# Performance work log

Hardware: AMD Instinct MI355X
Metric: run time of the kernel (lower is better)

Reference implementation:

```python
import jax, jax.numpy as jnp
import numpy as np

B, C, NQ, K, H, CAM, FFN = 2, 128, 200, 24000, 8, 16, 256

def setup_inputs() -> dict:
    key = jax.random.key(0)
    ks = jax.random.split(key, 32)
    def n(i, shape, scale=1.0):
        return jax.random.normal(ks[i], shape, dtype=jnp.float32) * scale
    return {
        "query_feat": n(0, (B, C, NQ)),
        "key_feat": n(1, (B, C, K)),
        "query_pos": jax.random.uniform(ks[2], (B, NQ, 2), dtype=jnp.float32),
        "key_pos": jax.random.uniform(ks[3], (B, K, 2), dtype=jnp.float32),
        "query_size": jax.random.uniform(ks[4], (B, NQ, 2), dtype=jnp.float32, minval=0.02, maxval=0.3),
        "cam_info": n(5, (B, CAM, K)),
        "Wproj_q": n(6, (C, C), 0.05), "Wproj_k": n(7, (C, C), 0.05),
        "Wq_pos1": n(8, (2, C), 0.5), "Wq_pos2": n(9, (C, C), 0.05),
        "Wk_pos1": n(10, (2, C), 0.5), "Wk_pos2": n(11, (C, C), 0.05),
        "Wsq": n(12, (C, C), 0.05), "Wsk": n(13, (C, C), 0.05),
        "Wsv": n(14, (C, C), 0.05), "Wso": n(15, (C, C), 0.05),
        "Wcq": n(16, (C, C), 0.05), "Wck": n(17, (C, C), 0.05),
        "Wcv": n(18, (C, C), 0.05), "Wco": n(19, (C, C), 0.05),
        "Wffn1": n(20, (C, FFN), 0.05), "bffn1": jnp.zeros((FFN,), jnp.float32),
        "Wffn2": n(21, (FFN, C), 0.05), "bffn2": jnp.zeros((C,), jnp.float32),
        "cam_w1": n(22, (CAM, C), 0.1), "cam_w2": n(23, (C, C), 0.05), "cam_w3": n(24, (C, C), 0.05),
    }

def _ln(x):
    m = x.mean(-1, keepdims=True)
    v = x.var(-1, keepdims=True)
    return (x - m) * jax.lax.rsqrt(v + 1e-5)

def _mha(q, k, v, Wq, Wk, Wv, Wo, bias=None):
    b, nq, c = q.shape
    dh = c // H
    qh = (q @ Wq).reshape(b, nq, H, dh)
    kh = (k @ Wk).reshape(b, k.shape[1], H, dh)
    vh = (v @ Wv).reshape(b, v.shape[1], H, dh)
    s = jnp.einsum('bqhd,bkhd->bhqk', qh, kh) * (1.0 / np.sqrt(dh))
    if bias is not None:
        s = s + bias[:, None]  # SMCA gaussian modulation, shared over heads
    a = jax.nn.softmax(s, axis=-1)
    o = jnp.einsum('bhqk,bkhd->bqhd', a, vh).reshape(b, nq, c)
    return o @ Wo

def reference(query_feat, key_feat, query_pos, key_pos, query_size, cam_info,
              Wproj_q, Wproj_k, Wq_pos1, Wq_pos2, Wk_pos1, Wk_pos2,
              Wsq, Wsk, Wsv, Wso, Wcq, Wck, Wcv, Wco,
              Wffn1, bffn1, Wffn2, bffn2, cam_w1, cam_w2, cam_w3):
    # 1x1-conv projections (img_projection / pts_projection)
    q = jnp.einsum('bcn,cd->bnd', query_feat, Wproj_q)   # [B,NQ,C]
    kf = jnp.einsum('bck,cd->bkd', key_feat, Wproj_k)    # [B,K,C]
    mu = cam_info.mean(axis=(0, 2), keepdims=True)
    var = cam_info.var(axis=(0, 2), keepdims=True)
    cb = (cam_info - mu) * jax.lax.rsqrt(var + 1e-5)     # [B,16,K]
    h = jax.nn.relu(jnp.einsum('bck,cd->bdk', cb, cam_w1))
    h = jax.nn.relu(jnp.einsum('bck,cd->bdk', h, cam_w2))
    gate = jax.nn.sigmoid(jnp.einsum('bck,cd->bdk', h, cam_w3))  # [B,C,K]
    kf = kf * gate.transpose(0, 2, 1)
    # learned position embeddings (MLP on normalized 2D coords)
    qpe = jax.nn.relu(query_pos @ Wq_pos1) @ Wq_pos2     # [B,NQ,C]
    kpe = jax.nn.relu(key_pos @ Wk_pos1) @ Wk_pos2       # [B,K,C]
    # self-attention over queries
    x = q
    xs = x + qpe
    x = _ln(x + _mha(xs, xs, x, Wsq, Wsk, Wsv, Wso))
    # SMCA gaussian attention bias: -|p_k - p_q|^2 / (2 sigma^2) per axis
    sigma = query_size * 0.5 + 1e-2                      # [B,NQ,2]
    diff = key_pos[:, None] - query_pos[:, :, None]      # [B,NQ,K,2]
    bias = -jnp.sum(diff * diff / (2.0 * (sigma * sigma)[:, :, None]), axis=-1)  # [B,NQ,K]
    # cross-attention with SMCA modulation
    x = _ln(x + _mha(x + qpe, kf + kpe, kf, Wcq, Wck, Wcv, Wco, bias))
    # FFN
    x = _ln(x + (jax.nn.relu(x @ Wffn1 + bffn1) @ Wffn2 + bffn2))
    return x  # [B,NQ,C]
```

## Files before the change

kernel.cpp:

```cpp
#include <hip/hip_runtime.h>
#include <math.h>

#define BB 2
#define CC 128
#define NQ 200
#define NQP 224
#define KK 24000
#define NH 8
#define DH 16
#define NCAM 16
#define NFFN 256

#define NSEG 50
#define TPS 15
#define NGRP (BB*NSEG)
#define SLOTX 13

#define TK 64
#define NPS (BB*NQP)
#define NQB (BB*NQ)

#define LOG2E 1.44269504f

#if __has_builtin(__builtin_amdgcn_exp2f)
#define EXP2(x) __builtin_amdgcn_exp2f(x)
#else
#define EXP2(x) exp2f(x)
#endif

#define O_MU    0
#define O_RSTD  16
#define O_SINV  32
#define O_CP    1024
#define O_Q0    2048
#define O_QPE   (O_Q0  + BB*NQ*CC)
#define O_XS    (O_QPE + BB*NQ*CC)
#define O_SQ    (O_XS  + BB*NQ*CC)
#define O_SK    (O_SQ  + BB*NQ*CC)
#define O_SV    (O_SK  + BB*NQ*CC)
#define O_SO    (O_SV  + BB*NQ*CC)
#define O_X1    (O_SO  + BB*NQ*CC)
#define O_OH    (O_X1  + BB*NQ*CC)
#define O_PART  (O_OH  + BB*NQ*CC)
#define O_BF    (O_PART + BB*NH*NSEG*NQP*18)

#define U_KH   0
#define U_VH   (BB*KK*CC)
#define U_FT   (2*BB*KK*CC)
#define U_CT   (3*BB*KK*CC)
#define U_W    (3*BB*KK*CC + BB*KK*32)
#define U_QW   (U_W + 4096 + 6*16384)
#define U_ONES (U_QW + BB*NQP*CC)
#define U_WX   (U_ONES + KK + 64)

typedef __attribute__((ext_vector_type(8))) short bfrag8;
typedef __attribute__((ext_vector_type(4))) float f32x4;
typedef __attribute__((ext_vector_type(16))) float f32x16;

__device__ __forceinline__ unsigned short f2bf(float x) {
    unsigned u = __float_as_uint(x);
    u += 0x7fffu + ((u >> 16) & 1u);
    return (unsigned short)(u >> 16);
}
__device__ __forceinline__ float bf2f(unsigned short h) {
    return __uint_as_float(((unsigned)h) << 16);
}
__device__ __forceinline__ unsigned cvtpk_bf16(float lo, float hi) {
    unsigned r;
    asm volatile("v_cvt_pk_bf16_f32 %0, %1, %2" : "=v"(r) : "v"(lo), "v"(hi));
    return r;
}
__device__ __forceinline__ void pl32swap(unsigned &a, unsigned &b) {
    asm volatile("v_permlane32_swap_b32 %0, %1" : "+v"(a), "+v"(b));
}

__device__ __forceinline__ float lnorm512(float x, int t, float* rs, float* rs2, float* col) {
    if (t < 128) { rs[t] = x; rs2[t] = x*x; }
    __syncthreads();
    if (t < 64) {
        float v  = rs[t]  + rs[t+64];
        float v2 = rs2[t] + rs2[t+64];
#pragma unroll
        for (int off = 32; off > 0; off >>= 1) {
            v  += __shfl_down(v,  off);
            v2 += __shfl_down(v2, off);
        }
        if (t == 0) { col[0] = v; col[1] = v2; }
    }
    __syncthreads();
    float mean = col[0] * (1.0f/128.0f);
    float var  = col[1] * (1.0f/128.0f) - mean*mean;
    return (x - mean) * rsqrtf(var + 1e-5f);
}


__global__ __launch_bounds__(512) void k_pre(
    const float* __restrict__ cam,
    const float* __restrict__ cw2, const float* __restrict__ cw3,
    const float* __restrict__ proj, const float* __restrict__ k2,
    const float* __restrict__ ck,  const float* __restrict__ cv,
    const float* __restrict__ cw1,
    unsigned short* __restrict__ wtU, unsigned short* __restrict__ onesU,
    unsigned short* __restrict__ wxU,
    float* __restrict__ ws,
    const float* __restrict__ qf, const float* __restrict__ qpos,
    const float* __restrict__ qsize,
    const float* __restrict__ Wpq, const float* __restrict__ Wp1,
    const float* __restrict__ Wp2,
    const float* __restrict__ Wsq, const float* __restrict__ Wsk,
    const float* __restrict__ Wsv)
{
    __shared__ float r1[256], r2[256];
    __shared__ float qrow[CC], ph[CC], xsr[CC], q0r[CC];
    __shared__ float pA[4*132], pB[4*132], pC[4*132];
    __shared__ float wckL[128*16];
    int t = threadIdx.x;
    if (blockIdx.x < 256) {
        int blk = blockIdx.x;
        int r = blk >> 3;
        int s = blk & 7;
        const float* src = cam + (size_t)r*KK + s*3000;
        float sm = 0.f, s2 = 0.f;
        if (t < 256)
            for (int i = t; i < 3000; i += 256) { float v = src[i]; sm += v; s2 += v*v; }
        if (t < 256) { r1[t] = sm; r2[t] = s2; }
        __syncthreads();
        for (int off = 128; off > 0; off >>= 1) {
            if (t < off) { r1[t] += r1[t+off]; r2[t] += r2[t+off]; }
            __syncthreads();
        }
        if (t == 0) { ws[O_CP + blk*2] = r1[0]; ws[O_CP + blk*2 + 1] = r2[0]; }
    } else if (blockIdx.x < 264) {
        int blk = blockIdx.x - 256;
        if (blk < 6) {
            const float* W = (blk==0)?cw2:(blk==1)?cw3:(blk==2)?proj:(blk==3)?k2:(blk==4)?ck:cv;
            unsigned short* dst = wtU + 4096 + blk*16384;
            for (int i = t; i < 16384; i += 512) {
                int j = i & 7, lx = (i >> 3) & 63, cs = (i >> 9) & 3, w16 = i >> 11;
                int d = w16*16 + (lx & 15);
                int c = cs*32 + (lx >> 4)*8 + j;
                dst[i] = f2bf(W[c*CC + d]);
            }
        } else if (blk == 6) {
            for (int i = t; i < 4096; i += 512) {
                int j = i & 7, lx = (i >> 3) & 63, w16 = i >> 9;
                int d = w16*16 + (lx & 15);
                int c = (lx >> 4)*8 + j;
                wtU[i] = (c < 16) ? f2bf(cw1[c*CC + d]) : (unsigned short)0;
            }
        } else {
            for (int i = t; i < KK + 64; i += 512) onesU[i] = 0x3F80;
        }
    } else if (blockIdx.x < 264 + NQB) {
        int row = blockIdx.x - 264;
        int b = row / NQ, n = row - b*NQ;
        int d = t & 127, p = t >> 7;
        if (t < CC) {
            qrow[t] = qf[((size_t)b*CC + t)*NQ + n];
            float px = qpos[row*2], py = qpos[row*2+1];
            ph[t] = fmaxf(px*Wp1[t] + py*Wp1[CC+t], 0.f);
        }
        if (t < 2) {
            float sg = qsize[row*2 + t]*0.5f + 0.01f;
            ws[O_SINV + row*2 + t] = LOG2E / (2.f * sg * sg);
        }
        __syncthreads();
        {
            float aQ = 0.f, aP = 0.f;
            int c0 = p*32;
#pragma unroll
            for (int c = 0; c < 32; c++) {
                aQ = fmaf(qrow[c0+c], Wpq[(c0+c)*CC + d], aQ);
                aP = fmaf(ph[c0+c],   Wp2[(c0+c)*CC + d], aP);
            }
            pA[p*132 + d] = aQ; pB[p*132 + d] = aP;
        }
        __syncthreads();
        if (t < CC) {
            float q0 = (pA[t] + pA[132+t]) + (pA[264+t] + pA[396+t]);
            float pe = (pB[t] + pB[132+t]) + (pB[264+t] + pB[396+t]);
            ws[O_Q0  + row*CC + t] = q0;
            ws[O_QPE + row*CC + t] = pe;
            q0r[t] = q0;
            xsr[t] = q0 + pe;
        }
        __syncthreads();
        {
            float a = 0.f, k2v = 0.f, v2 = 0.f;
            int c0 = p*32;
#pragma unroll
            for (int c = 0; c < 32; c++) {
                float xv = xsr[c0+c], qv = q0r[c0+c];
                a   = fmaf(xv, Wsq[(c0+c)*CC + d], a);
                k2v = fmaf(xv, Wsk[(c0+c)*CC + d], k2v);
                v2  = fmaf(qv, Wsv[(c0+c)*CC + d], v2);
            }
            pA[p*132 + d] = a; pB[p*132 + d] = k2v; pC[p*132 + d] = v2;
        }
        __syncthreads();
        if (t < CC) {
            ws[O_SQ + row*CC + t] = (pA[t] + pA[132+t]) + (pA[264+t] + pA[396+t]);
            ws[O_SK + row*CC + t] = (pB[t] + pB[132+t]) + (pB[264+t] + pB[396+t]);
            ws[O_SV + row*CC + t] = (pC[t] + pC[132+t]) + (pC[264+t] + pC[396+t]);
        }
    } else {
        int w16 = blockIdx.x - (264 + NQB);
        {
            int e = t >> 2, i0 = (t & 3) * 4;
#pragma unroll
            for (int i = 0; i < 4; i++)
                wckL[e*16 + i0 + i] = ck[(size_t)e*CC + w16*16 + i0 + i];
        }
        __syncthreads();
        {
            int c = t >> 2, dls = (t & 3) * 4;
            const float* wrow = k2 + (size_t)c*CC;
            float acc[4] = {0.f, 0.f, 0.f, 0.f};
            for (int e = 0; e < 128; e++) {
                float w = wrow[e];
#pragma unroll
                for (int i = 0; i < 4; i++)
                    acc[i] = fmaf(w, wckL[e*16 + dls + i], acc[i]);
            }
            int cs = c >> 5, j = c & 7, lhi = ((c >> 3) & 3) * 16;
#pragma unroll
            for (int i = 0; i < 4; i++) {
                int lane = lhi + (dls + i);
                wxU[((w16*4 + cs) << 9) + lane*8 + j] = f2bf(acc[i]);
            }
        }
    }
}


__device__ __forceinline__ int frag_col(int d0, int m) {
    return ((((d0 >> 5) * 4 + ((d0 >> 3) & 3)) * 16 + m) << 3) + (d0 & 7);
}

__device__ __forceinline__ void ld_a4h(bfrag8 a[4], const unsigned short* __restrict__ Wf,
                                       int w16, int l) {
#pragma unroll
    for (int cs = 0; cs < 4; cs++)
        a[cs] = *(const bfrag8*)(Wf + ((w16*4 + cs) << 9) + l*8);
}

__device__ __forceinline__ void mfma_apply4h(const unsigned short* __restrict__ X,
                                             const bfrag8 a[4],
                                             int l, f32x4 acc[4])
{
    const f32x4 z = {0.f, 0.f, 0.f, 0.f};
#pragma unroll
    for (int kt = 0; kt < 4; kt++) acc[kt] = z;
#pragma unroll
    for (int kt = 0; kt < 4; kt++)
#pragma unroll
        for (int cs = 0; cs < 4; cs++) {
            bfrag8 bf = *(const bfrag8*)(X + ((kt*4 + cs) << 9) + l*8);
            acc[kt] = __builtin_amdgcn_mfma_f32_16x16x32_bf16(a[cs], bf, acc[kt], 0, 0, 0);
        }
}

__device__ __forceinline__ void mfma_acc4h(const unsigned short* __restrict__ X,
                                           const bfrag8 a[4],
                                           int l, f32x4 acc[4])
{
#pragma unroll
    for (int kt = 0; kt < 4; kt++)
#pragma unroll
        for (int cs = 0; cs < 4; cs++) {
            bfrag8 bf = *(const bfrag8*)(X + ((kt*4 + cs) << 9) + l*8);
            acc[kt] = __builtin_amdgcn_mfma_f32_16x16x32_bf16(a[cs], bf, acc[kt], 0, 0, 0);
        }
}

__device__ __forceinline__ void mfma_apply1h(const unsigned short* __restrict__ X,
                                             bfrag8 a1, int l, f32x4 acc[4])
{
    const f32x4 z = {0.f, 0.f, 0.f, 0.f};
#pragma unroll
    for (int kt = 0; kt < 4; kt++) acc[kt] = z;
#pragma unroll
    for (int kt = 0; kt < 4; kt++) {
        bfrag8 bf = *(const bfrag8*)(X + (kt << 11) + l*8);
        acc[kt] = __builtin_amdgcn_mfma_f32_16x16x32_bf16(a1, bf, acc[kt], 0, 0, 0);
    }
}

template<bool RELU>
__device__ __forceinline__ void store_tiles_h(unsigned short* __restrict__ Xd,
                                              const f32x4 acc[4], int m, int g, int dbase)
{
    int cp = frag_col(dbase + g*4, m);
#pragma unroll
    for (int kt = 0; kt < 4; kt++) {
        ushort4 pk;
        float v0 = acc[kt][0], v1 = acc[kt][1], v2 = acc[kt][2], v3 = acc[kt][3];
        if (RELU) { v0 = fmaxf(v0,0.f); v1 = fmaxf(v1,0.f); v2 = fmaxf(v2,0.f); v3 = fmaxf(v3,0.f); }
        pk.x = f2bf(v0); pk.y = f2bf(v1); pk.z = f2bf(v2); pk.w = f2bf(v3);
        *(ushort4*)(Xd + (kt << 11) + cp) = pk;
    }
}


__global__ __launch_bounds__(512) void k_chainps(
    const float* __restrict__ key_feat, const float* __restrict__ cam_info,
    const float* __restrict__ key_pos, const float* __restrict__ Wk1,
    const unsigned short* __restrict__ wtU, const unsigned short* __restrict__ wxU,
    unsigned short* __restrict__ khH, unsigned short* __restrict__ vhH,
    const float* __restrict__ Wso, const float* __restrict__ Wcq,
    unsigned short* __restrict__ qwU,
    float* __restrict__ ws)
{
    __shared__ __align__(16) union SM {
        struct {
            unsigned short XA[8192];
            unsigned short XB[8192];
            float w1buf[256];
            float kpx[TK], kpy[TK];
            float cmu[NCAM], crs[NCAM];
        } c;
        struct {
            float sor[CC], qcr[CC], sq[CC];
            float part[4*132];
            float rs[CC], rs2[CC], col[2];
        } s;
    } sm;

    int t = threadIdx.x;

    if (blockIdx.x < NPS) {
        int row = blockIdx.x;
        int b = row / NQP, n = row - b*NQP;
        if (n >= NQ) { if (t < CC) qwU[(size_t)row*CC + t] = 0; return; }
        int rw = b*NQ + n;
        int d = t & 127, p = t >> 7;
        float* sor = sm.s.sor;
        float* qcr = sm.s.qcr;
        float* sq  = sm.s.sq;
        float* part = sm.s.part;
        float* rs = sm.s.rs;
        float* rs2 = sm.s.rs2;
        float* col = sm.s.col;

        if (t < CC) sq[t] = ws[O_SQ + (size_t)rw*CC + t];
        __syncthreads();

        {
            int h = t >> 6;
            int l = t & 63;
            float qv[16];
#pragma unroll
            for (int j = 0; j < 16; j++) qv[j] = sq[h*16 + j];
            float s[4], pexp[4];
            float mloc = -1e30f;
#pragma unroll
            for (int w2 = 0; w2 < 4; w2++) {
                int k = l + w2*64;
                float sv = -1e30f;
                if (k < NQ) {
                    const float* kr = ws + O_SK + ((size_t)(b*NQ + k))*CC + h*16;
                    float a2 = 0.f;
#pragma unroll
                    for (int j = 0; j < 16; j += 4) {
                        float4 kv = *(const float4*)(kr + j);
                        a2 += qv[j]*kv.x + qv[j+1]*kv.y + qv[j+2]*kv.z + qv[j+3]*kv.w;
                    }
                    sv = a2 * 0.25f;
                }
                s[w2] = sv;
                mloc = fmaxf(mloc, sv);
            }
#pragma unroll
            for (int off = 32; off > 0; off >>= 1) mloc = fmaxf(mloc, __shfl_xor(mloc, off));
            float lsum = 0.f;
#pragma unroll
            for (int w2 = 0; w2 < 4; w2++) {
                pexp[w2] = (s[w2] > -1e29f) ? __expf(s[w2] - mloc) : 0.f;
                lsum += pexp[w2];
            }
#pragma unroll
            for (int off = 32; off > 0; off >>= 1) lsum += __shfl_xor(lsum, off);
            float o[16];
#pragma unroll
            for (int j = 0; j < 16; j++) o[j] = 0.f;
#pragma unroll
            for (int w2 = 0; w2 < 4; w2++) {
                int k = l + w2*64;
                if (k < NQ) {
                    const float* vr = ws + O_SV + ((size_t)(b*NQ + k))*CC + h*16;
                    float pw = pexp[w2];
#pragma unroll
                    for (int j = 0; j < 16; j += 4) {
                        float4 vv = *(const float4*)(vr + j);
                        o[j]   = fmaf(pw, vv.x, o[j]);
                        o[j+1] = fmaf(pw, vv.y, o[j+1]);
                        o[j+2] = fmaf(pw, vv.z, o[j+2]);
                        o[j+3] = fmaf(pw, vv.w, o[j+3]);
                    }
                }
            }
#pragma unroll
            for (int j = 0; j < 16; j++) {
#pragma unroll
                for (int off = 32; off > 0; off >>= 1) o[j] += __shfl_xor(o[j], off);
            }
            if (l == 0) {
                float inv = 1.f / lsum;
#pragma unroll
                for (int j = 0; j < 16; j++) sor[h*16 + j] = o[j] * inv;
            }
        }
        __syncthreads();

        {
            float acc = 0.f;
            int c0 = p*32;
#pragma unroll
            for (int c = 0; c < 32; c++) acc = fmaf(sor[c0+c], Wso[(c0+c)*CC + d], acc);
            part[p*132 + d] = acc;
        }
        __syncthreads();
        float x = 0.f;
        if (t < CC) x = ws[O_Q0 + rw*CC + t] + ((part[t] + part[132+t]) + (part[264+t] + part[396+t]));
        x = lnorm512(x, t, rs, rs2, col);
        if (t < CC) {
            ws[O_X1 + rw*CC + t] = x;
            qcr[t] = x + ws[O_QPE + rw*CC + t];
        }
        __syncthreads();
        {
            float acc = 0.f;
            int c0 = p*32;
#pragma unroll
            for (int c = 0; c < 32; c++) acc = fmaf(qcr[c0+c], Wcq[(c0+c)*CC + d], acc);
            part[p*132 + d] = acc;
        }
        __syncthreads();
        if (t < CC) {
            float qh = (part[t] + part[132+t]) + (part[264+t] + part[396+t]);
            qwU[(size_t)row*CC + t] = f2bf(0.25f * LOG2E * qh);
        }
        return;
    }

    unsigned short* XA = sm.c.XA;
    unsigned short* XB = sm.c.XB;
    float* w1buf = sm.c.w1buf;
    float* kpx = sm.c.kpx;
    float* kpy = sm.c.kpy;
    float* cmu = sm.c.cmu;
    float* crs = sm.c.crs;

    int blk = blockIdx.x - NPS;
    int b = blk / (KK/TK);
    int k0 = (blk - b*(KK/TK)) * TK;
    int l = t & 63;
    int m = l & 15, g = l >> 4;
    int w16 = t >> 6;
    int dbase = w16 * 16;

    const unsigned short* WT_CW1  = wtU;
    const unsigned short* WT_CW2  = wtU + 4096;
    const unsigned short* WT_CW3  = wtU + 4096 + 16384;
    const unsigned short* WT_PROJ = wtU + 4096 + 2*16384;
    const unsigned short* WT_CK   = wtU + 4096 + 4*16384;
    const unsigned short* WT_CV   = wtU + 4096 + 5*16384;

    if (t < NCAM) {
        float S = 0.f, S2 = 0.f;
#pragma unroll
        for (int bb2 = 0; bb2 < BB; bb2++)
#pragma unroll
            for (int s = 0; s < 8; s++) {
                int blk2 = ((bb2*NCAM + t) << 3) | s;
                S  += ws[O_CP + blk2*2];
                S2 += ws[O_CP + blk2*2 + 1];
            }
        float mu  = S * (1.0f/(BB*KK));
        float var = S2 * (1.0f/(BB*KK)) - mu*mu;
        cmu[t] = mu;
        crs[t] = rsqrtf(var + 1e-5f);
    }
    __syncthreads();

    if (t < 256) {
        int c = t >> 4;
        int kq = (t & 15) * 4;
        float4 v = *(const float4*)(cam_info + ((size_t)b*NCAM + c)*KK + k0 + kq);
        float mu = cmu[c], rsd = crs[c];
        int ktb = (kq >> 4) << 11;
        int cb  = frag_col(c & ~7, 0) + (c & 7);
        XA[ktb + cb + ((kq  ) & 15)*8] = f2bf((v.x - mu)*rsd);
        XA[ktb + cb + ((kq+1) & 15)*8] = f2bf((v.y - mu)*rsd);
        XA[ktb + cb + ((kq+2) & 15)*8] = f2bf((v.z - mu)*rsd);
        XA[ktb + cb + ((kq+3) & 15)*8] = f2bf((v.w - mu)*rsd);
        {
            int z = t;
            int kt = z >> 6, r = z & 63;
            int gz = 2 + (r >> 5), mz = (r >> 1) & 15, j4 = (r & 1) * 4;
            ushort4 z4 = make_ushort4(0,0,0,0);
            *(ushort4*)(XA + (kt << 11) + (gz*16 + mz)*8 + j4) = z4;
        }
        w1buf[t] = Wk1[t];
    }
    if (t < TK) {
        float2 p = ((const float2*)key_pos)[b*KK + k0 + t];
        kpx[t] = p.x; kpy[t] = p.y;
    }

    bfrag8 a1 = *(const bfrag8*)(WT_CW1 + (w16 << 9) + l*8);
    bfrag8 aA[4], aB[4], aC[4];
    ld_a4h(aA, WT_CW2, w16, l);
    __syncthreads();

    f32x4 acc[4];

    mfma_apply1h(XA, a1, l, acc);
    store_tiles_h<true>(XB, acc, m, g, dbase);
    __syncthreads();
    ld_a4h(aB, WT_CW3, w16, l);

    mfma_apply4h(XB, aA, l, acc);
    store_tiles_h<true>(XA, acc, m, g, dbase);
    __syncthreads();
    ld_a4h(aA, WT_PROJ, w16, l);

    {
        int c = t >> 2, q4 = t & 3;
        const float* src = key_feat + ((size_t)b*CC + c)*KK + k0 + q4*16;
        int base = (q4 << 11) + frag_col(c & ~7, 0) + (c & 7);
#pragma unroll
        for (int qq = 0; qq < 4; qq++) {
            float4 v = ((const float4*)src)[qq];
            int mk = qq*4;
            XB[base + (mk  )*8] = f2bf(v.x);
            XB[base + (mk+1)*8] = f2bf(v.y);
            XB[base + (mk+2)*8] = f2bf(v.z);
            XB[base + (mk+3)*8] = f2bf(v.w);
        }
    }
    mfma_apply4h(XA, aB, l, acc);
    float garr[4][4];
#pragma unroll
    for (int kt = 0; kt < 4; kt++)
#pragma unroll
        for (int r = 0; r < 4; r++)
            garr[kt][r] = 1.f / (1.f + __expf(-acc[kt][r]));
    __syncthreads();
    ld_a4h(aB, WT_CK, w16, l);

    mfma_apply4h(XB, aA, l, acc);
#pragma unroll
    for (int kt = 0; kt < 4; kt++)
#pragma unroll
        for (int r = 0; r < 4; r++)
            acc[kt][r] *= garr[kt][r];
    store_tiles_h<false>(XA, acc, m, g, dbase);
    __syncthreads();
    ld_a4h(aA, WT_CV, w16, l);
    ld_a4h(aC, wxU, w16, l);

    {
        int k = t >> 3, dq = (t & 7) * 16;
        int ktb = (k >> 4) << 11;
        int mk = k & 15;
        float px = kpx[k], py = kpy[k];
        union { unsigned short u[8]; bfrag8 f; } cA, cB;
#pragma unroll
        for (int j = 0; j < 8; j++) {
            cA.u[j] = f2bf(fmaxf(px*w1buf[dq+j]   + py*w1buf[128+dq+j],   0.f));
            cB.u[j] = f2bf(fmaxf(px*w1buf[dq+8+j] + py*w1buf[128+dq+8+j], 0.f));
        }
        *(bfrag8*)(XB + ktb + frag_col(dq,     mk)) = cA.f;
        *(bfrag8*)(XB + ktb + frag_col(dq + 8, mk)) = cB.f;
    }
    __syncthreads();

    mfma_apply4h(XA, aB, l, acc);
    mfma_acc4h(XB, aC, l, acc);
#pragma unroll
    for (int kt = 0; kt < 4; kt++) {
        int k = k0 + kt*16 + m;
        ushort4 pk;
        pk.x = f2bf(acc[kt][0]); pk.y = f2bf(acc[kt][1]);
        pk.z = f2bf(acc[kt][2]); pk.w = f2bf(acc[kt][3]);
        *(ushort4*)(khH + (((size_t)(b*NH + w16)*KK + k) << 4) + g*4) = pk;
    }
    mfma_apply4h(XA, aA, l, acc);
#pragma unroll
    for (int kt = 0; kt < 4; kt++) {
        int k = k0 + kt*16 + m;
        size_t tb = ((size_t)(b*NH + w16)*(KK/32) + (k >> 5))*512 + (k & 31);
#pragma unroll
        for (int r = 0; r < 4; r++)
            vhH[tb + (g*4 + r)*32] = f2bf(acc[kt][r]);
    }
}


struct KPRegs { float4 r[8]; };

__device__ __forceinline__ void kp_read(KPRegs& kp, const float4* __restrict__ f4, int fb) {
#pragma unroll
    for (int mm = 0; mm < 4; mm++) {
        kp.r[2*mm]   = f4[fb + 4*mm];
        kp.r[2*mm+1] = f4[fb + 4*mm + 1];
    }
}
__device__ __forceinline__ void kp_bias(f32x16& bias, const KPRegs& kp,
                                        float qx, float qy, float nsx, float nsy) {
#pragma unroll
    for (int mm = 0; mm < 4; mm++) {
        float4 c0 = kp.r[2*mm], c1 = kp.r[2*mm+1];
        float dx, dy;
        dx = c0.x - qx; dy = c0.y - qy; bias[4*mm+0] = fmaf(dy*dy, nsy, dx*dx*nsx);
        dx = c0.z - qx; dy = c0.w - qy; bias[4*mm+1] = fmaf(dy*dy, nsy, dx*dx*nsx);
        dx = c1.x - qx; dy = c1.y - qy; bias[4*mm+2] = fmaf(dy*dy, nsy, dx*dx*nsx);
        dx = c1.z - qx; dy = c1.w - qy; bias[4*mm+3] = fmaf(dy*dy, nsy, dx*dx*nsx);
    }
}

__device__ __forceinline__ void flash_head(
    const f32x16& s, f32x16& acc, bfrag8 vfa, bfrag8 vfb)
{
    float p[16];
#pragma unroll
    for (int i = 0; i < 16; i++) p[i] = EXP2(s[i]);
    unsigned pk[8];
#pragma unroll
    for (int mm = 0; mm < 4; mm++) {
        pk[2*mm]   = cvtpk_bf16(p[4*mm],   p[4*mm+1]);
        pk[2*mm+1] = cvtpk_bf16(p[4*mm+2], p[4*mm+3]);
    }
    {
        unsigned a0 = pk[0], b0 = pk[2];
        unsigned a1 = pk[1], b1 = pk[3];
        pl32swap(a0, b0);
        pl32swap(a1, b1);
        union { unsigned u[4]; bfrag8 f; } pf;
        pf.u[0] = a0; pf.u[1] = a1; pf.u[2] = b0; pf.u[3] = b1;
        acc = __builtin_amdgcn_mfma_f32_32x32x16_bf16(vfa, pf.f, acc, 0, 0, 0);
    }
    {
        unsigned a0 = pk[4], b0 = pk[6];
        unsigned a1 = pk[5], b1 = pk[7];
        pl32swap(a0, b0);
        pl32swap(a1, b1);
        union { unsigned u[4]; bfrag8 f; } pf;
        pf.u[0] = a0; pf.u[1] = a1; pf.u[2] = b0; pf.u[3] = b1;
        acc = __builtin_amdgcn_mfma_f32_32x32x16_bf16(vfb, pf.f, acc, 0, 0, 0);
    }
}

__global__ __launch_bounds__(256) void k_flash(
    const float* __restrict__ qpos, const float* __restrict__ key_pos,
    const unsigned short* __restrict__ khH, const unsigned short* __restrict__ vhH,
    const unsigned short* __restrict__ qwU, const unsigned short* __restrict__ onesU,
    float* __restrict__ ws)
{
    int id = blockIdx.x;
    int slot = id >> 3;
    int group = (id & 7) * SLOTX + slot / 7;
    if (group >= NGRP) return;
    int qt  = slot % 7;
    int b   = group / NSEG;
    int seg = group - b*NSEG;

    int wv  = threadIdx.x >> 6;
    int l   = threadIdx.x & 63;
    int lq  = l & 31;
    int g   = l >> 5;
    int h0  = wv*2, h1 = h0 + 1;
    int q   = qt*32 + lq;
    int qc  = min(q, NQ-1);
    int t   = threadIdx.x;

    __shared__ __align__(16) float kpbuf[TPS*32*2];

    int kt0 = seg * (TPS*32);
    {
        const float4* src = (const float4*)(key_pos + ((size_t)b*KK + kt0)*2);
        for (int i = t; i < TPS*32/2; i += 256)
            ((float4*)kpbuf)[i] = src[i];
    }

    float qx  = qpos[(b*NQ+qc)*2], qy = qpos[(b*NQ+qc)*2+1];
    float nsx = -ws[O_SINV + (b*NQ+qc)*2];
    float nsy = -ws[O_SINV + (b*NQ+qc)*2+1];

    const unsigned short* qrow = qwU + ((size_t)b*NQP + q)*CC + g*8;
    bfrag8 qf0 = *(const bfrag8*)(qrow + h0*DH);
    bfrag8 qf1 = *(const bfrag8*)(qrow + h1*DH);

    const unsigned short* kb0 = khH + (((size_t)(b*NH + h0)*KK + lq) << 4) + g*8;
    const unsigned short* kb1 = khH + (((size_t)(b*NH + h1)*KK + lq) << 4) + g*8;
    bool isOnes = (lq == 16);
    const unsigned short* vt0 = vhH + (size_t)(b*NH + h0)*(KK/32)*512 + (lq & 15)*32 + g*8;
    const unsigned short* vt1 = vhH + (size_t)(b*NH + h1)*(KK/32)*512 + (lq & 15)*32 + g*8;
    const unsigned short* on8 = onesU + g*8;

    f32x16 acc0, acc1;
#pragma unroll
    for (int i = 0; i < 16; i++) { acc0[i] = 0.f; acc1[i] = 0.f; }

    int tile0 = kt0 >> 5;
    bfrag8 kf0 = *(const bfrag8*)(kb0 + ((size_t)kt0 << 4));
    bfrag8 kf1 = *(const bfrag8*)(kb1 + ((size_t)kt0 << 4));
    bfrag8 vc00 = isOnes ? *(const bfrag8*)on8 : *(const bfrag8*)(vt0 + (size_t)tile0*512);
    bfrag8 vc01 = isOnes ? *(const bfrag8*)on8 : *(const bfrag8*)(vt0 + (size_t)tile0*512 + 16);
    bfrag8 vc10 = isOnes ? *(const bfrag8*)on8 : *(const bfrag8*)(vt1 + (size_t)tile0*512);
    bfrag8 vc11 = isOnes ? *(const bfrag8*)on8 : *(const bfrag8*)(vt1 + (size_t)tile0*512 + 16);

    __syncthreads();

    const float4* kpf4 = (const float4*)kpbuf;
    KPRegs kpn;
    kp_read(kpn, kpf4, 2*g);
    f32x16 bias;
    kp_bias(bias, kpn, qx, qy, nsx, nsy);

    for (int it = 0; it < TPS; it++) {
        int itn = (it+1 < TPS) ? it+1 : it;
        int kn = kt0 + itn*32;
        int tn = kn >> 5;
        bfrag8 kf0n = *(const bfrag8*)(kb0 + ((size_t)kn << 4));
        bfrag8 kf1n = *(const bfrag8*)(kb1 + ((size_t)kn << 4));
        bfrag8 vn00 = isOnes ? *(const bfrag8*)on8 : *(const bfrag8*)(vt0 + (size_t)tn*512);
        bfrag8 vn01 = isOnes ? *(const bfrag8*)on8 : *(const bfrag8*)(vt0 + (size_t)tn*512 + 16);
        bfrag8 vn10 = isOnes ? *(const bfrag8*)on8 : *(const bfrag8*)(vt1 + (size_t)tn*512);
        bfrag8 vn11 = isOnes ? *(const bfrag8*)on8 : *(const bfrag8*)(vt1 + (size_t)tn*512 + 16);
        kp_read(kpn, kpf4, itn*16 + 2*g);

        f32x16 s0 = __builtin_amdgcn_mfma_f32_32x32x16_bf16(kf0, qf0, bias, 0, 0, 0);
        f32x16 s1 = __builtin_amdgcn_mfma_f32_32x32x16_bf16(kf1, qf1, bias, 0, 0, 0);

        flash_head(s0, acc0, vc00, vc01);
        flash_head(s1, acc1, vc10, vc11);

        kp_bias(bias, kpn, qx, qy, nsx, nsy);
        kf0 = kf0n; kf1 = kf1n;
        vc00 = vn00; vc01 = vn01; vc10 = vn10; vc11 = vn11;
    }

    {
        float* o = ws + O_PART + (((size_t)(b*NH + h0)*NSEG + seg)*NQP + q)*18;
        if (l < 32) o[0] = acc0[8];
#pragma unroll
        for (int rr = 0; rr < 8; rr++) o[1 + (rr&3) + 8*(rr>>2) + 4*g] = acc0[rr];
    }
    {
        float* o = ws + O_PART + (((size_t)(b*NH + h1)*NSEG + seg)*NQP + q)*18;
        if (l < 32) o[0] = acc1[8];
#pragma unroll
        for (int rr = 0; rr < 8; rr++) o[1 + (rr&3) + 8*(rr>>2) + 4*g] = acc1[rr];
    }
}


__global__ __launch_bounds__(512) void k_final(
    const float* __restrict__ Wco, const float* __restrict__ W1,
    const float* __restrict__ b1f, const float* __restrict__ W2,
    const float* __restrict__ b2f, float* __restrict__ ws,
    float* __restrict__ out)
{
    int row = blockIdx.x;
    int b = row / NQ, q = row - b*NQ;
    int t = threadIdx.x;
    int d = t & 127, p = t >> 7;
    __shared__ float orow[CC], x1r[CC], x2r[CC], hrr[NFFN];
    __shared__ float part[4*132];
    __shared__ float part2[2*260];
    __shared__ float rs[CC], rs2[CC], col[2];
    __shared__ float lpart[32], Lh[8];

    {
        int h = d >> 4, j = d & 15;
        const float* pb = ws + O_PART + (((size_t)(b*NH + h)*NSEG)*NQP + q)*18;
        int s0 = p*13, s1 = (s0 + 13 < NSEG) ? s0 + 13 : NSEG;
        float sA = 0.f, sL = 0.f;
        for (int sg = s0; sg < s1; sg++) {
            const float* pp = pb + (size_t)sg*(NQP*18);
            sA += pp[1 + j];
            if (j == 0) sL += pp[0];
        }
        part[p*132 + d] = sA;
        if (j == 0) lpart[p*8 + h] = sL;
    }
    if (t < CC) x1r[t] = ws[O_X1 + (size_t)row*CC + t];
    __syncthreads();
    if (t < 8) Lh[t] = (lpart[t] + lpart[8+t]) + (lpart[16+t] + lpart[24+t]);
    __syncthreads();
    if (t < CC)
        orow[t] = ((part[t] + part[132+t]) + (part[264+t] + part[396+t])) / Lh[t >> 4];
    __syncthreads();

    {
        float acc = 0.f;
        int c0 = p*32;
#pragma unroll
        for (int c = 0; c < 32; c++) acc = fmaf(orow[c0+c], Wco[(c0+c)*CC + d], acc);
        part[p*132 + d] = acc;
    }
    __syncthreads();
    float x = 0.f;
    if (t < CC) x = x1r[t] + ((part[t] + part[132+t]) + (part[264+t] + part[396+t]));
    x = lnorm512(x, t, rs, rs2, col);
    if (t < CC) x2r[t] = x;
    __syncthreads();
    {
        int o = t & 255, ph2 = t >> 8;
        float h = 0.f;
        int c0 = ph2*64;
#pragma unroll 16
        for (int c = 0; c < 64; c++) h = fmaf(x2r[c0+c], W1[(c0+c)*NFFN + o], h);
        part2[ph2*260 + o] = h;
    }
    __syncthreads();
    if (t < NFFN) hrr[t] = fmaxf(part2[t] + part2[260+t] + b1f[t], 0.f);
    __syncthreads();
    {
        float acc = 0.f;
        int f0 = p*64;
#pragma unroll 16
        for (int f = 0; f < 64; f++) acc = fmaf(hrr[f0+f], W2[(f0+f)*CC + d], acc);
        part[p*132 + d] = acc;
    }
    __syncthreads();
    float y = 0.f;
    if (t < CC) y = x2r[t] + b2f[t] + ((part[t] + part[132+t]) + (part[264+t] + part[396+t]));
    y = lnorm512(y, t, rs, rs2, col);
    if (t < CC) out[(size_t)row*CC + t] = y;
}


extern "C" void kernel_launch(void* const* d_in, const int* in_sizes, int n_in,
                              void* d_out, int out_size, void* d_ws, size_t ws_size,
                              hipStream_t stream)
{
    const float* query_feat = (const float*)d_in[0];
    const float* key_feat   = (const float*)d_in[1];
    const float* query_pos  = (const float*)d_in[2];
    const float* key_pos    = (const float*)d_in[3];
    const float* query_size = (const float*)d_in[4];
    const float* cam_info   = (const float*)d_in[5];
    const float* Wproj_q = (const float*)d_in[6];
    const float* Wproj_k = (const float*)d_in[7];
    const float* Wq_pos1 = (const float*)d_in[8];
    const float* Wq_pos2 = (const float*)d_in[9];
    const float* Wk_pos1 = (const float*)d_in[10];
    const float* Wk_pos2 = (const float*)d_in[11];
    const float* Wsq = (const float*)d_in[12];
    const float* Wsk = (const float*)d_in[13];
    const float* Wsv = (const float*)d_in[14];
    const float* Wso = (const float*)d_in[15];
    const float* Wcq = (const float*)d_in[16];
    const float* Wck = (const float*)d_in[17];
    const float* Wcv = (const float*)d_in[18];
    const float* Wco = (const float*)d_in[19];
    const float* Wffn1 = (const float*)d_in[20];
    const float* bffn1 = (const float*)d_in[21];
    const float* Wffn2 = (const float*)d_in[22];
    const float* bffn2 = (const float*)d_in[23];
    const float* cam_w1 = (const float*)d_in[24];
    const float* cam_w2 = (const float*)d_in[25];
    const float* cam_w3 = (const float*)d_in[26];
    float* ws  = (float*)d_ws;
    float* out = (float*)d_out;
    unsigned short* wsu = (unsigned short*)(ws + O_BF);
    unsigned short* khH = wsu + U_KH;
    unsigned short* vhH = wsu + U_VH;
    unsigned short* wtU = wsu + U_W;
    unsigned short* qwU = wsu + U_QW;
    unsigned short* onU = wsu + U_ONES;
    unsigned short* wxU = wsu + U_WX;

    hipLaunchKernelGGL(k_pre, dim3(264 + NQB + 8), dim3(512), 0, stream,
        cam_info, cam_w2, cam_w3, Wproj_k, Wk_pos2, Wck, Wcv, cam_w1, wtU, onU, wxU, ws,
        query_feat, query_pos, query_size, Wproj_q, Wq_pos1, Wq_pos2, Wsq, Wsk, Wsv);
    hipLaunchKernelGGL(k_chainps, dim3(NPS + BB*KK/TK), dim3(512), 0, stream,
        key_feat, cam_info, key_pos, Wk_pos1, wtU, wxU, khH, vhH, Wso, Wcq, qwU, ws);
    hipLaunchKernelGGL(k_flash, dim3(8*SLOTX*7), dim3(256), 0, stream,
        query_pos, key_pos, khH, vhH, qwU, onU, ws);
    hipLaunchKernelGGL(k_final, dim3(BB*NQ), dim3(512), 0, stream,
        Wco, Wffn1, bffn1, Wffn2, bffn2, ws, out);
}
```

Baseline: 103.7 us.

## Warp-specialize key projection: 4 MFMA waves compute two tiles, loader waves stage inputs

Restructures the per-key-tile projection block so that the first 4 waves each compute two 16-column output slices via MFMA, while the remaining 4 waves load cam_info, key_feat and position embeddings into LDS in parallel. The B-operand fragments are loaded from LDS once into registers and reused across both output slices, which cuts LDS read traffic. The cost is higher register pressure (16 bfrag8 plus gate arrays held per thread) and compute concentrated on half the waves, which may lower occupancy or leave the MFMA units underused.

Measured after the change: 113.4 us. 9.3% more time.

```diff
diff --git a/kernel.cpp b/kernel.cpp
--- a/kernel.cpp
+++ b/kernel.cpp
@@ -244,13 +244,25 @@
         a[cs] = *(const bfrag8*)(Wf + ((w16*4 + cs) << 9) + l*8);
 }
 
-__device__ __forceinline__ void mfma_apply4h(const unsigned short* __restrict__ X,
-                                             const bfrag8 a[4],
-                                             int l, f32x4 acc[4])
-{
+__device__ __forceinline__ void ld_x16(bfrag8 xb[16], const unsigned short* __restrict__ X, int l) {
+#pragma unroll
+    for (int i = 0; i < 16; i++)
+        xb[i] = *(const bfrag8*)(X + (i << 9) + l*8);
+}
+
+__device__ __forceinline__ void mfma_x(const bfrag8 xb[16], const bfrag8 a[4], f32x4 acc[4]) {
     const f32x4 z = {0.f, 0.f, 0.f, 0.f};
 #pragma unroll
     for (int kt = 0; kt < 4; kt++) acc[kt] = z;
+#pragma unroll
+    for (int kt = 0; kt < 4; kt++)
+#pragma unroll
+        for (int cs = 0; cs < 4; cs++)
+            acc[kt] = __builtin_amdgcn_mfma_f32_16x16x32_bf16(a[cs], xb[kt*4+cs], acc[kt], 0, 0, 0);
+}
+
+__device__ __forceinline__ void mfma_acc_lds(const unsigned short* __restrict__ X,
+                                             const bfrag8 a[4], int l, f32x4 acc[4]) {
 #pragma unroll
     for (int kt = 0; kt < 4; kt++)
 #pragma unroll
@@ -258,32 +270,6 @@
             bfrag8 bf = *(const bfrag8*)(X + ((kt*4 + cs) << 9) + l*8);
             acc[kt] = __builtin_amdgcn_mfma_f32_16x16x32_bf16(a[cs], bf, acc[kt], 0, 0, 0);
         }
-}
-
-__device__ __forceinline__ void mfma_acc4h(const unsigned short* __restrict__ X,
-                                           const bfrag8 a[4],
-                                           int l, f32x4 acc[4])
-{
-#pragma unroll
-    for (int kt = 0; kt < 4; kt++)
-#pragma unroll
-        for (int cs = 0; cs < 4; cs++) {
-            bfrag8 bf = *(const bfrag8*)(X + ((kt*4 + cs) << 9) + l*8);
-            acc[kt] = __builtin_amdgcn_mfma_f32_16x16x32_bf16(a[cs], bf, acc[kt], 0, 0, 0);
-        }
-}
-
-__device__ __forceinline__ void mfma_apply1h(const unsigned short* __restrict__ X,
-                                             bfrag8 a1, int l, f32x4 acc[4])
-{
-    const f32x4 z = {0.f, 0.f, 0.f, 0.f};
-#pragma unroll
-    for (int kt = 0; kt < 4; kt++) acc[kt] = z;
-#pragma unroll
-    for (int kt = 0; kt < 4; kt++) {
-        bfrag8 bf = *(const bfrag8*)(X + (kt << 11) + l*8);
-        acc[kt] = __builtin_amdgcn_mfma_f32_16x16x32_bf16(a1, bf, acc[kt], 0, 0, 0);
-    }
 }
 
 template<bool RELU>
@@ -456,8 +442,8 @@
     int k0 = (blk - b*(KK/TK)) * TK;
     int l = t & 63;
     int m = l & 15, g = l >> 4;
-    int w16 = t >> 6;
-    int dbase = w16 * 16;
+    int wv = t >> 6;
+    int ts = t - 256;
 
     const unsigned short* WT_CW1  = wtU;
     const unsigned short* WT_CW2  = wtU + 4096;
@@ -483,117 +469,203 @@
     }
     __syncthreads();
 
-    if (t < 256) {
-        int c = t >> 4;
-        int kq = (t & 15) * 4;
-        float4 v = *(const float4*)(cam_info + ((size_t)b*NCAM + c)*KK + k0 + kq);
-        float mu = cmu[c], rsd = crs[c];
-        int ktb = (kq >> 4) << 11;
-        int cb  = frag_col(c & ~7, 0) + (c & 7);
-        XA[ktb + cb + ((kq  ) & 15)*8] = f2bf((v.x - mu)*rsd);
-        XA[ktb + cb + ((kq+1) & 15)*8] = f2bf((v.y - mu)*rsd);
-        XA[ktb + cb + ((kq+2) & 15)*8] = f2bf((v.z - mu)*rsd);
-        XA[ktb + cb + ((kq+3) & 15)*8] = f2bf((v.w - mu)*rsd);
-        {
-            int z = t;
-            int kt = z >> 6, r = z & 63;
+    if (t >= 256) {
+        {
+            int c = ts >> 4;
+            int kq = (ts & 15) * 4;
+            float4 v = *(const float4*)(cam_info + ((size_t)b*NCAM + c)*KK + k0 + kq);
+            float mu = cmu[c], rsd = crs[c];
+            int ktb = (kq >> 4) << 11;
+            int cb  = frag_col(c & ~7, 0) + (c & 7);
+            XA[ktb + cb + ((kq  ) & 15)*8] = f2bf((v.x - mu)*rsd);
+            XA[ktb + cb + ((kq+1) & 15)*8] = f2bf((v.y - mu)*rsd);
+            XA[ktb + cb + ((kq+2) & 15)*8] = f2bf((v.z - mu)*rsd);
+            XA[ktb + cb + ((kq+3) & 15)*8] = f2bf((v.w - mu)*rsd);
+        }
+        {
+            int kt = ts >> 6, r = ts & 63;
             int gz = 2 + (r >> 5), mz = (r >> 1) & 15, j4 = (r & 1) * 4;
             ushort4 z4 = make_ushort4(0,0,0,0);
             *(ushort4*)(XA + (kt << 11) + (gz*16 + mz)*8 + j4) = z4;
         }
-        w1buf[t] = Wk1[t];
-    }
-    if (t < TK) {
-        float2 p = ((const float2*)key_pos)[b*KK + k0 + t];
-        kpx[t] = p.x; kpy[t] = p.y;
-    }
-
-    bfrag8 a1 = *(const bfrag8*)(WT_CW1 + (w16 << 9) + l*8);
-    bfrag8 aA[4], aB[4], aC[4];
-    ld_a4h(aA, WT_CW2, w16, l);
-    __syncthreads();
-
-    f32x4 acc[4];
-
-    mfma_apply1h(XA, a1, l, acc);
-    store_tiles_h<true>(XB, acc, m, g, dbase);
-    __syncthreads();
-    ld_a4h(aB, WT_CW3, w16, l);
-
-    mfma_apply4h(XB, aA, l, acc);
-    store_tiles_h<true>(XA, acc, m, g, dbase);
-    __syncthreads();
-    ld_a4h(aA, WT_PROJ, w16, l);
-
-    {
-        int c = t >> 2, q4 = t & 3;
-        const float* src = key_feat + ((size_t)b*CC + c)*KK + k0 + q4*16;
-        int base = (q4 << 11) + frag_col(c & ~7, 0) + (c & 7);
-#pragma unroll
-        for (int qq = 0; qq < 4; qq++) {
-            float4 v = ((const float4*)src)[qq];
-            int mk = qq*4;
-            XB[base + (mk  )*8] = f2bf(v.x);
-            XB[base + (mk+1)*8] = f2bf(v.y);
-            XB[base + (mk+2)*8] = f2bf(v.z);
-            XB[base + (mk+3)*8] = f2bf(v.w);
-        }
-    }
-    mfma_apply4h(XA, aB, l, acc);
-    float garr[4][4];
-#pragma unroll
-    for (int kt = 0; kt < 4; kt++)
-#pragma unroll
-        for (int r = 0; r < 4; r++)
-            garr[kt][r] = 1.f / (1.f + __expf(-acc[kt][r]));
-    __syncthreads();
-    ld_a4h(aB, WT_CK, w16, l);
-
-    mfma_apply4h(XB, aA, l, acc);
-#pragma unroll
-    for (int kt = 0; kt < 4; kt++)
-#pragma unroll
-        for (int r = 0; r < 4; r++)
-            acc[kt][r] *= garr[kt][r];
-    store_tiles_h<false>(XA, acc, m, g, dbase);
-    __syncthreads();
-    ld_a4h(aA, WT_CV, w16, l);
-    ld_a4h(aC, wxU, w16, l);
-
-    {
-        int k = t >> 3, dq = (t & 7) * 16;
+        w1buf[ts] = Wk1[ts];
+        if (ts < TK) {
+            float2 p = ((const float2*)key_pos)[b*KK + k0 + ts];
+            kpx[ts] = p.x; kpy[ts] = p.y;
+        }
+    }
+    __syncthreads();
+
+    float garrA[4][4], garrB[4][4];
+
+    if (t < 256) {
+        bfrag8 xc[4];
+#pragma unroll
+        for (int kt = 0; kt < 4; kt++)
+            xc[kt] = *(const bfrag8*)(XA + (kt << 11) + l*8);
+#pragma unroll
+        for (int s = 0; s < 2; s++) {
+            int w16 = wv + s*4;
+            bfrag8 a1 = *(const bfrag8*)(WT_CW1 + (w16 << 9) + l*8);
+            f32x4 acc[4];
+            const f32x4 z = {0.f,0.f,0.f,0.f};
+#pragma unroll
+            for (int kt = 0; kt < 4; kt++) acc[kt] = z;
+#pragma unroll
+            for (int kt = 0; kt < 4; kt++)
+                acc[kt] = __builtin_amdgcn_mfma_f32_16x16x32_bf16(a1, xc[kt], acc[kt], 0, 0, 0);
+            store_tiles_h<true>(XB, acc, m, g, w16*16);
+        }
+    }
+    __syncthreads();
+
+    if (t < 256) {
+        bfrag8 xb[16];
+        ld_x16(xb, XB, l);
+#pragma unroll
+        for (int s = 0; s < 2; s++) {
+            int w16 = wv + s*4;
+            bfrag8 aA[4];
+            ld_a4h(aA, WT_CW2, w16, l);
+            f32x4 acc[4];
+            mfma_x(xb, aA, acc);
+            store_tiles_h<true>(XA, acc, m, g, w16*16);
+        }
+    }
+    __syncthreads();
+
+    if (t < 256) {
+        bfrag8 xb[16];
+        ld_x16(xb, XA, l);
+        {
+            bfrag8 aA[4];
+            ld_a4h(aA, WT_CW3, wv, l);
+            f32x4 acc[4];
+            mfma_x(xb, aA, acc);
+#pragma unroll
+            for (int kt = 0; kt < 4; kt++)
+#pragma unroll
+                for (int r = 0; r < 4; r++)
+                    garrA[kt][r] = 1.f / (1.f + __expf(-acc[kt][r]));
+        }
+        {
+            bfrag8 aA[4];
+            ld_a4h(aA, WT_CW3, wv + 4, l);
+            f32x4 acc[4];
+            mfma_x(xb, aA, acc);
+#pragma unroll
+            for (int kt = 0; kt < 4; kt++)
+#pragma unroll
+                for (int r = 0; r < 4; r++)
+                    garrB[kt][r] = 1.f / (1.f + __expf(-acc[kt][r]));
+        }
+    } else {
+        int c = ts >> 1, hf = ts & 1;
+        int cb = frag_col(c & ~7, 0) + (c & 7);
+        const float* srcc = key_feat + ((size_t)b*CC + c)*KK + k0;
+#pragma unroll
+        for (int q4i = 0; q4i < 2; q4i++) {
+            int kt2 = hf*2 + q4i;
+            const float4* src = (const float4*)(srcc + kt2*16);
+            int base = (kt2 << 11) + cb;
+#pragma unroll
+            for (int qq = 0; qq < 4; qq++) {
+                float4 v = src[qq];
+                int mk = qq*4;
+                XB[base + (mk  )*8] = f2bf(v.x);
+                XB[base + (mk+1)*8] = f2bf(v.y);
+                XB[base + (mk+2)*8] = f2bf(v.z);
+                XB[base + (mk+3)*8] = f2bf(v.w);
+            }
+        }
+    }
+    __syncthreads();
+
+    if (t < 256) {
+        bfrag8 xb[16];
+        ld_x16(xb, XB, l);
+        {
+            bfrag8 aA[4];
+            ld_a4h(aA, WT_PROJ, wv, l);
+            f32x4 acc[4];
+            mfma_x(xb, aA, acc);
+#pragma unroll
+            for (int kt = 0; kt < 4; kt++)
+#pragma unroll
+                for (int r = 0; r < 4; r++)
+                    acc[kt][r] *= garrA[kt][r];
+            store_tiles_h<false>(XA, acc, m, g, wv*16);
+        }
+        {
+            bfrag8 aA[4];
+            ld_a4h(aA, WT_PROJ, wv + 4, l);
+            f32x4 acc[4];
+            mfma_x(xb, aA, acc);
+#pragma unroll
+            for (int kt = 0; kt < 4; kt++)
+#pragma unroll
+                for (int r = 0; r < 4; r++)
+                    acc[kt][r] *= garrB[kt][r];
+            store_tiles_h<false>(XA, acc, m, g, (wv+4)*16);
+        }
+    }
+    __syncthreads();
+
+    bfrag8 xkf[16];
+    if (t < 256) {
+        ld_x16(xkf, XA, l);
+#pragma unroll
+        for (int s = 0; s < 2; s++) {
+            int w16 = wv + s*4;
+            bfrag8 aA[4];
+            ld_a4h(aA, WT_CV, w16, l);
+            f32x4 acc[4];
+            mfma_x(xkf, aA, acc);
+#pragma unroll
+            for (int kt = 0; kt < 4; kt++) {
+                int k = k0 + kt*16 + m;
+                size_t tb = ((size_t)(b*NH + w16)*(KK/32) + (k >> 5))*512 + (k & 31);
+#pragma unroll
+                for (int r = 0; r < 4; r++)
+                    vhH[tb + (g*4 + r)*32] = f2bf(acc[kt][r]);
+            }
+        }
+    } else {
+        int k = ts >> 2, dq0 = (ts & 3) * 32;
         int ktb = (k >> 4) << 11;
         int mk = k & 15;
         float px = kpx[k], py = kpy[k];
-        union { unsigned short u[8]; bfrag8 f; } cA, cB;
-#pragma unroll
-        for (int j = 0; j < 8; j++) {
-            cA.u[j] = f2bf(fmaxf(px*w1buf[dq+j]   + py*w1buf[128+dq+j],   0.f));
-            cB.u[j] = f2bf(fmaxf(px*w1buf[dq+8+j] + py*w1buf[128+dq+8+j], 0.f));
-        }
-        *(bfrag8*)(XB + ktb + frag_col(dq,     mk)) = cA.f;
-        *(bfrag8*)(XB + ktb + frag_col(dq + 8, mk)) = cB.f;
-    }
-    __syncthreads();
-
-    mfma_apply4h(XA, aB, l, acc);
-    mfma_acc4h(XB, aC, l, acc);
-#pragma unroll
-    for (int kt = 0; kt < 4; kt++) {
-        int k = k0 + kt*16 + m;
-        ushort4 pk;
-        pk.x = f2bf(acc[kt][0]); pk.y = f2bf(acc[kt][1]);
-        pk.z = f2bf(acc[kt][2]); pk.w = f2bf(acc[kt][3]);
-        *(ushort4*)(khH + (((size_t)(b*NH + w16)*KK + k) << 4) + g*4) = pk;
-    }
-    mfma_apply4h(XA, aA, l, acc);
-#pragma unroll
-    for (int kt = 0; kt < 4; kt++) {
-        int k = k0 + kt*16 + m;
-        size_t tb = ((size_t)(b*NH + w16)*(KK/32) + (k >> 5))*512 + (k & 31);
-#pragma unroll
-        for (int r = 0; r < 4; r++)
-            vhH[tb + (g*4 + r)*32] = f2bf(acc[kt][r]);
+#pragma unroll
+        for (int i = 0; i < 4; i++) {
+            int dq = dq0 + i*8;
+            union { unsigned short u[8]; bfrag8 f; } cA;
+#pragma unroll
+            for (int j = 0; j < 8; j++)
+                cA.u[j] = f2bf(fmaxf(px*w1buf[dq+j] + py*w1buf[128+dq+j], 0.f));
+            *(bfrag8*)(XB + ktb + frag_col(dq, mk)) = cA.f;
+        }
+    }
+    __syncthreads();
+
+    if (t < 256) {
+#pragma unroll
+        for (int s = 0; s < 2; s++) {
+            int w16 = wv + s*4;
+            bfrag8 aA[4], aC[4];
+            ld_a4h(aA, WT_CK, w16, l);
+            ld_a4h(aC, wxU, w16, l);
+            f32x4 acc[4];
+            mfma_x(xkf, aA, acc);
+            mfma_acc_lds(XB, aC, l, acc);
+#pragma unroll
+            for (int kt = 0; kt < 4; kt++) {
+                int k = k0 + kt*16 + m;
+                ushort4 pk;
+                pk.x = f2bf(acc[kt][0]); pk.y = f2bf(acc[kt][1]);
+                pk.z = f2bf(acc[kt][2]); pk.w = f2bf(acc[kt][3]);
+                *(ushort4*)(khH + (((size_t)(b*NH + w16)*KK + k) << 4) + g*4) = pk;
+            }
+        }
     }
 }
 
```
